# Kernel tuning notes

Measured on AMD Instinct MI355X. Metric: run time of the kernel, lower is better.

Reference implementation:

```python
import jax, jax.numpy as jnp
import numpy as np

N_NODES = 100000
N_EDGES = 3200000
IN_F = 256
OUT_F = 128
NEG_SLOPE = 0.2


def setup_inputs() -> dict:
    key = jax.random.key(0)
    k1, k2, k3, k4, k5 = jax.random.split(key, 5)
    features = jax.random.normal(k1, (N_NODES, IN_F), dtype=jnp.float32)
    # xavier-uniform-ish linear weight [out, in]
    limit = float(np.sqrt(6.0 / (IN_F + OUT_F)))
    weight = jax.random.uniform(k2, (OUT_F, IN_F), dtype=jnp.float32, minval=-limit, maxval=limit)
    edge_vals = jax.random.uniform(k3, (N_EDGES,), dtype=jnp.float32)
    edge_rows = jax.random.randint(k4, (N_EDGES,), 0, N_NODES, dtype=jnp.int32)
    edge_cols = jax.random.randint(k5, (N_EDGES,), 0, N_NODES, dtype=jnp.int32)
    return {"features": features, "weight": weight, "edge_vals": edge_vals,
            "edge_rows": edge_rows, "edge_cols": edge_cols}


def reference(features, weight, edge_vals, edge_rows, edge_cols):
    # support = LeakyReLU(features @ W^T)   (active=True path)
    support = jax.nn.leaky_relu(jnp.einsum('ni,oi->no', features, weight), NEG_SLOPE)
    # output = spmm(adj, support): out[r] += v_e * support[c_e]
    gathered = support[edge_cols] * edge_vals[:, None]   # [E, out]
    out = jax.ops.segment_sum(gathered, edge_rows, num_segments=N_NODES)
    return out
```

## Files before the change

### kernel.cpp

```cpp
#include <hip/hip_runtime.h>
#include <hip/hip_bf16.h>

#define N_NODES 100000
#define N_EDGES 3200000
#define IN_F 256
#define OUT_F 128
#define NEG_SLOPE 0.2f
#define NB 782
#define CHUNK 4096
#define NPB 782
#define BCAP 4608

typedef short s16x8 __attribute__((ext_vector_type(8)));
typedef float f32x4 __attribute__((ext_vector_type(4)));
typedef float f32x2v __attribute__((ext_vector_type(2)));
typedef unsigned u32x2 __attribute__((ext_vector_type(2)));

__device__ __forceinline__ unsigned short f2bf(float f) {
    __bf16 h = (__bf16)f;
    return __builtin_bit_cast(unsigned short, h);
}
__device__ __forceinline__ float bf2f(unsigned short u) {
    unsigned int x = ((unsigned int)u) << 16;
    return __builtin_bit_cast(float, x);
}

__global__ void wcvt_kernel(const float* __restrict__ w, unsigned short* __restrict__ wb) {
    int t = blockIdx.x * blockDim.x + threadIdx.x;
    if (t >= (OUT_F / 16) * (IN_F / 32) * 64) return;
    int lane = t & 63;
    int nt   = (t >> 6) & 7;
    int kit  = t >> 9;
    int l16  = lane & 15;
    int quad = lane >> 4;
    const float* src = w + (nt * 16 + l16) * IN_F + kit * 32 + quad * 8;
    float4 v0 = *(const float4*)src;
    float4 v1 = *(const float4*)(src + 4);
    ushort4 o0, o1;
    o0.x = f2bf(v0.x); o0.y = f2bf(v0.y); o0.z = f2bf(v0.z); o0.w = f2bf(v0.w);
    o1.x = f2bf(v1.x); o1.y = f2bf(v1.y); o1.z = f2bf(v1.z); o1.w = f2bf(v1.w);
    *(ushort4*)(wb + t * 8)     = o0;
    *(ushort4*)(wb + t * 8 + 4) = o1;
}

__global__ __launch_bounds__(256) void gemm_kernel(
    const float* __restrict__ feat, const unsigned short* __restrict__ wb,
    unsigned short* __restrict__ sup) {
    int wid  = threadIdx.x >> 6;
    int lane = threadIdx.x & 63;
    long m0 = ((long)blockIdx.x * 4 + wid) * 16;
    if (m0 >= N_NODES) return;
    int quad = lane >> 4;
    int l16  = lane & 15;
    int kq   = quad * 8;

    const float* arow = feat + (m0 + l16) * IN_F + kq;

    f32x4 acc[8];
#pragma unroll
    for (int nt = 0; nt < 8; ++nt) acc[nt] = (f32x4){0.f, 0.f, 0.f, 0.f};

#pragma unroll
    for (int k0 = 0; k0 < IN_F; k0 += 32) {
        f32x4 a0 = __builtin_nontemporal_load((const f32x4*)(arow + k0));
        f32x4 a1 = __builtin_nontemporal_load((const f32x4*)(arow + k0 + 4));
        s16x8 a;
        a[0] = (short)f2bf(a0[0]); a[1] = (short)f2bf(a0[1]);
        a[2] = (short)f2bf(a0[2]); a[3] = (short)f2bf(a0[3]);
        a[4] = (short)f2bf(a1[0]); a[5] = (short)f2bf(a1[1]);
        a[6] = (short)f2bf(a1[2]); a[7] = (short)f2bf(a1[3]);
        const unsigned short* wp = wb + (k0 >> 5) * 4096 + lane * 8;
#pragma unroll
        for (int nt = 0; nt < 8; ++nt) {
            s16x8 b = *(const s16x8*)(wp + nt * 512);
            acc[nt] = __builtin_amdgcn_mfma_f32_16x16x32_bf16(a, b, acc[nt], 0, 0, 0);
        }
    }

    int crow = (int)m0 + quad * 4;
#pragma unroll
    for (int nt = 0; nt < 8; ++nt) {
#pragma unroll
        for (int r = 0; r < 4; ++r) {
            float v = acc[nt][r];
            v = (v > 0.f) ? v : (NEG_SLOPE * v);
            sup[(long)(crow + r) * OUT_F + nt * 16 + l16] = f2bf(v);
        }
    }
}

__global__ __launch_bounds__(256) void hist_kernel(const int* __restrict__ rows,
                                                   int* __restrict__ gcnt) {
    __shared__ int lh[NB];
    int t = threadIdx.x;
    for (int s = t; s < NB; s += 256) lh[s] = 0;
    __syncthreads();
    int e0 = blockIdx.x * CHUNK;
    int m = N_EDGES - e0; if (m > CHUNK) m = CHUNK;
    for (int k = t; k < m; k += 256)
        atomicAdd(&lh[__builtin_nontemporal_load(rows + e0 + k) >> 7], 1);
    __syncthreads();
    for (int s = t; s < NB; s += 256)
        gcnt[s * NPB + blockIdx.x] = lh[s];
}

__global__ __launch_bounds__(256) void scan_kernel(int* __restrict__ gcnt,
                                                   int* __restrict__ bcnt) {
    __shared__ int st[256];
    int s = blockIdx.x, t = threadIdx.x;
    int* row = gcnt + (long)s * NPB;
    int v[4]; int sum = 0;
#pragma unroll
    for (int k = 0; k < 4; ++k) {
        int i = t * 4 + k;
        v[k] = (i < NPB) ? row[i] : 0;
        sum += v[k];
    }
    st[t] = sum;
    __syncthreads();
    for (int o = 1; o < 256; o <<= 1) {
        int x = (t >= o) ? st[t - o] : 0;
        __syncthreads();
        st[t] += x;
        __syncthreads();
    }
    int run = st[t] - sum;
#pragma unroll
    for (int k = 0; k < 4; ++k) {
        int i = t * 4 + k;
        if (i < NPB) row[i] = run;
        run += v[k];
    }
    if (t == 255) bcnt[s] = run;
}

__global__ __launch_bounds__(256) void mscatter_kernel(const int* __restrict__ rows,
    const int* __restrict__ cols, const float* __restrict__ vals,
    const int* __restrict__ boff, uint2* __restrict__ ed) {
    __shared__ uint2 stage[CHUNK];
    __shared__ unsigned short sbkt[CHUNK];
    __shared__ int lhist[NB];
    __shared__ int lbase[NB];
    __shared__ int st[256];
    int t = threadIdx.x;
    for (int s = t; s < NB; s += 256) lhist[s] = 0;
    __syncthreads();
    int e0 = blockIdx.x * CHUNK;
    int m = N_EDGES - e0; if (m > CHUNK) m = CHUNK;

    int rk[16]; int rr[16]; unsigned cw[16], vw[16];
#pragma unroll
    for (int k = 0; k < 16; ++k) {
        int i = k * 256 + t;
        if (i < m) {
            int e = e0 + i;
            int r = __builtin_nontemporal_load(rows + e);
            rr[k] = r;
            cw[k] = (unsigned)__builtin_nontemporal_load(cols + e);
            vw[k] = __builtin_bit_cast(unsigned, __builtin_nontemporal_load(vals + e));
            rk[k] = atomicAdd(&lhist[r >> 7], 1);
        }
    }
    __syncthreads();
    for (int s = t; s < NB; s += 256)
        lbase[s] = boff[(long)s * NPB + blockIdx.x];
    int base = t * 4; int sum = 0; int hv[4];
#pragma unroll
    for (int k = 0; k < 4; ++k) {
        int s = base + k;
        hv[k] = (s < NB) ? lhist[s] : 0;
        sum += hv[k];
    }
    st[t] = sum;
    __syncthreads();
    for (int o = 1; o < 256; o <<= 1) {
        int x = (t >= o) ? st[t - o] : 0;
        __syncthreads();
        st[t] += x;
        __syncthreads();
    }
    int run = st[t] - sum;
#pragma unroll
    for (int k = 0; k < 4; ++k) {
        int s = base + k;
        if (s < NB) lhist[s] = run;
        run += hv[k];
    }
    __syncthreads();
#pragma unroll
    for (int k = 0; k < 16; ++k) {
        int i = k * 256 + t;
        if (i < m) {
            int r  = rr[k];
            int b  = r >> 7;
            int rl = r & 127;
            int pos = lhist[b] + rk[k];
            stage[pos].x = ((unsigned)rl << 17) | cw[k];
            stage[pos].y = vw[k];
            sbkt[pos] = (unsigned short)b;
        }
    }
    __syncthreads();
    for (int i = t; i < m; i += 256) {
        int b = sbkt[i];
        int g = lbase[b] + (i - lhist[b]);
        if (g < BCAP) ed[(long)b * BCAP + g] = stage[i];
    }
}

__global__ __launch_bounds__(1024) void gather_kernel(const uint2* __restrict__ ed,
    const int* __restrict__ bcnt,
    const unsigned short* __restrict__ sup, float* __restrict__ out, int b0) {
    __shared__ uint2 stage[BCAP];
    __shared__ int h[128];
    __shared__ int bs[128];
    __shared__ int cur[128];
    int t = threadIdx.x;
    int bkt = b0 + blockIdx.x;
    if (t < 128) h[t] = 0;
    __syncthreads();
    int n = bcnt[bkt]; if (n > BCAP) n = BCAP;
    const uint2* p = ed + (long)bkt * BCAP;

    uint2 er[5];
#pragma unroll
    for (int k = 0; k < 5; ++k) {
        int i = k * 1024 + t;
        if (i < n) {
            u32x2 v = __builtin_nontemporal_load((const u32x2*)(p + i));
            er[k].x = v[0]; er[k].y = v[1];
        }
    }
#pragma unroll
    for (int k = 0; k < 5; ++k) {
        int i = k * 1024 + t;
        if (i < n) atomicAdd(&h[er[k].x >> 17], 1);
    }
    __syncthreads();

    if (t < 128) bs[t] = h[t];
    __syncthreads();
    for (int o = 1; o < 128; o <<= 1) {
        int v = 0;
        if (t < 128 && t >= o) v = bs[t - o];
        __syncthreads();
        if (t < 128) bs[t] += v;
        __syncthreads();
    }
    if (t < 128) {
        int excl = bs[t] - h[t];
        bs[t] = excl;
        cur[t] = excl;
    }
    __syncthreads();

#pragma unroll
    for (int k = 0; k < 5; ++k) {
        int i = k * 1024 + t;
        if (i < n) {
            int rl = er[k].x >> 17;
            int pos = atomicAdd(&cur[rl], 1);
            stage[pos] = er[k];
        }
    }
    __syncthreads();

    int wid = t >> 6, lane = t & 63;
    long rowbase = (long)bkt * 128;

#define PROC(E) {                                                            \
        int col = (E).x & 0x1FFFF;                                           \
        float v = __builtin_bit_cast(float, (E).y);                          \
        ushort2 s2 = *(const ushort2*)(sup + (long)col * OUT_F + lane * 2);  \
        a0 += v * bf2f(s2.x); a1 += v * bf2f(s2.y);                          \
    }

    for (int rq = 0; rq < 8; ++rq) {
        int lr = wid * 8 + rq;
        int s0 = bs[lr];
        int mm = h[lr];
        float a0 = 0.f, a1 = 0.f;
        int i = 0;
        for (; i + 16 <= mm; i += 16) {
            uint2 e[16];
#pragma unroll
            for (int k = 0; k < 16; ++k) e[k] = stage[s0 + i + k];
#pragma unroll
            for (int k = 0; k < 16; ++k) PROC(e[k]);
        }
        for (; i + 8 <= mm; i += 8) {
            uint2 e0 = stage[s0 + i],     e1 = stage[s0 + i + 1];
            uint2 e2 = stage[s0 + i + 2], e3 = stage[s0 + i + 3];
            uint2 e4 = stage[s0 + i + 4], e5 = stage[s0 + i + 5];
            uint2 e6 = stage[s0 + i + 6], e7 = stage[s0 + i + 7];
            PROC(e0); PROC(e1); PROC(e2); PROC(e3);
            PROC(e4); PROC(e5); PROC(e6); PROC(e7);
        }
        for (; i < mm; ++i) { uint2 e0 = stage[s0 + i]; PROC(e0); }
        long grow = rowbase + lr;
        if (grow < N_NODES) {
            f32x2v f; f[0] = a0; f[1] = a1;
            __builtin_nontemporal_store(f, (f32x2v*)(out + grow * OUT_F + lane * 2));
        }
    }
#undef PROC
}

extern "C" void kernel_launch(void* const* d_in, const int* in_sizes, int n_in,
                              void* d_out, int out_size, void* d_ws, size_t ws_size,
                              hipStream_t stream) {
    const float* feat  = (const float*)d_in[0];
    const float* w     = (const float*)d_in[1];
    const float* evals = (const float*)d_in[2];
    const int*   erows = (const int*)d_in[3];
    const int*   ecols = (const int*)d_in[4];
    float* out = (float*)d_out;

    char* p = (char*)d_ws;
    unsigned short* wb  = (unsigned short*)p;  p += 65536;
    unsigned short* sup = (unsigned short*)p;  p += (size_t)N_NODES * OUT_F * 2;
    int* gcnt   = (int*)p;                     p += (size_t)NB * NPB * 4;
    int* bcnt   = (int*)p;                     p += 4096;
    uint2* ed   = (uint2*)p;

    wcvt_kernel<<<16, 256, 0, stream>>>(w, wb);

    int gemm_blocks = (N_NODES / 16 + 3) / 4;
    gemm_kernel<<<gemm_blocks, 256, 0, stream>>>(feat, wb, sup);

    hist_kernel<<<NPB, 256, 0, stream>>>(erows, gcnt);
    scan_kernel<<<NB, 256, 0, stream>>>(gcnt, bcnt);
    mscatter_kernel<<<NPB, 256, 0, stream>>>(erows, ecols, evals, gcnt, ed);

    int gh = NB / 2;
    gather_kernel<<<gh, 1024, 0, stream>>>(ed, bcnt, sup, out, 0);
    gather_kernel<<<NB - gh, 1024, 0, stream>>>(ed, bcnt, sup, out, gh);
}
```

Before: 388.4 us.

## Scatter edges directly to global buckets and shrink gather blocks to 512 threads

The multi-scatter kernel drops its shared-memory staging, local scan and second copy pass. Each edge is now written straight to its global bucket slot using its local atomic rank plus the bucket base offset, which removes LDS traffic and several barriers but turns the global writes into uncoalesced scattered stores. Separately, the gather kernel is retuned to 512 threads, with each thread holding 9 edges and each wave covering 16 rows. The gather launch is also split into four launches instead of two.

```diff
diff --git a/kernel.cpp b/kernel.cpp
--- a/kernel.cpp
+++ b/kernel.cpp
@@ -137,11 +137,8 @@
 __global__ __launch_bounds__(256) void mscatter_kernel(const int* __restrict__ rows,
     const int* __restrict__ cols, const float* __restrict__ vals,
     const int* __restrict__ boff, uint2* __restrict__ ed) {
-    __shared__ uint2 stage[CHUNK];
-    __shared__ unsigned short sbkt[CHUNK];
     __shared__ int lhist[NB];
     __shared__ int lbase[NB];
-    __shared__ int st[256];
     int t = threadIdx.x;
     for (int s = t; s < NB; s += 256) lhist[s] = 0;
     __syncthreads();
@@ -164,28 +161,6 @@
     __syncthreads();
     for (int s = t; s < NB; s += 256)
         lbase[s] = boff[(long)s * NPB + blockIdx.x];
-    int base = t * 4; int sum = 0; int hv[4];
-#pragma unroll
-    for (int k = 0; k < 4; ++k) {
-        int s = base + k;
-        hv[k] = (s < NB) ? lhist[s] : 0;
-        sum += hv[k];
-    }
-    st[t] = sum;
-    __syncthreads();
-    for (int o = 1; o < 256; o <<= 1) {
-        int x = (t >= o) ? st[t - o] : 0;
-        __syncthreads();
-        st[t] += x;
-        __syncthreads();
-    }
-    int run = st[t] - sum;
-#pragma unroll
-    for (int k = 0; k < 4; ++k) {
-        int s = base + k;
-        if (s < NB) lhist[s] = run;
-        run += hv[k];
-    }
     __syncthreads();
 #pragma unroll
     for (int k = 0; k < 16; ++k) {
@@ -193,22 +168,18 @@
         if (i < m) {
             int r  = rr[k];
             int b  = r >> 7;
-            int rl = r & 127;
-            int pos = lhist[b] + rk[k];
-            stage[pos].x = ((unsigned)rl << 17) | cw[k];
-            stage[pos].y = vw[k];
-            sbkt[pos] = (unsigned short)b;
-        }
-    }
-    __syncthreads();
-    for (int i = t; i < m; i += 256) {
-        int b = sbkt[i];
-        int g = lbase[b] + (i - lhist[b]);
-        if (g < BCAP) ed[(long)b * BCAP + g] = stage[i];
-    }
-}
-
-__global__ __launch_bounds__(1024) void gather_kernel(const uint2* __restrict__ ed,
+            int g  = lbase[b] + rk[k];
+            if (g < BCAP) {
+                uint2 e;
+                e.x = ((unsigned)(r & 127) << 17) | cw[k];
+                e.y = vw[k];
+                ed[(long)b * BCAP + g] = e;
+            }
+        }
+    }
+}
+
+__global__ __launch_bounds__(512) void gather_kernel(const uint2* __restrict__ ed,
     const int* __restrict__ bcnt,
     const unsigned short* __restrict__ sup, float* __restrict__ out, int b0) {
     __shared__ uint2 stage[BCAP];
@@ -222,18 +193,18 @@
     int n = bcnt[bkt]; if (n > BCAP) n = BCAP;
     const uint2* p = ed + (long)bkt * BCAP;
 
-    uint2 er[5];
-#pragma unroll
-    for (int k = 0; k < 5; ++k) {
-        int i = k * 1024 + t;
+    uint2 er[9];
+#pragma unroll
+    for (int k = 0; k < 9; ++k) {
+        int i = k * 512 + t;
         if (i < n) {
             u32x2 v = __builtin_nontemporal_load((const u32x2*)(p + i));
             er[k].x = v[0]; er[k].y = v[1];
         }
     }
 #pragma unroll
-    for (int k = 0; k < 5; ++k) {
-        int i = k * 1024 + t;
+    for (int k = 0; k < 9; ++k) {
+        int i = k * 512 + t;
         if (i < n) atomicAdd(&h[er[k].x >> 17], 1);
     }
     __syncthreads();
@@ -255,8 +226,8 @@
     __syncthreads();
 
 #pragma unroll
-    for (int k = 0; k < 5; ++k) {
-        int i = k * 1024 + t;
+    for (int k = 0; k < 9; ++k) {
+        int i = k * 512 + t;
         if (i < n) {
             int rl = er[k].x >> 17;
             int pos = atomicAdd(&cur[rl], 1);
@@ -275,8 +246,8 @@
         a0 += v * bf2f(s2.x); a1 += v * bf2f(s2.y);                          \
     }
 
-    for (int rq = 0; rq < 8; ++rq) {
-        int lr = wid * 8 + rq;
+    for (int rq = 0; rq < 16; ++rq) {
+        int lr = wid * 16 + rq;
         int s0 = bs[lr];
         int mm = h[lr];
         float a0 = 0.f, a1 = 0.f;
@@ -332,7 +303,9 @@
     scan_kernel<<<NB, 256, 0, stream>>>(gcnt, bcnt);
     mscatter_kernel<<<NPB, 256, 0, stream>>>(erows, ecols, evals, gcnt, ed);
 
-    int gh = NB / 2;
-    gather_kernel<<<gh, 1024, 0, stream>>>(ed, bcnt, sup, out, 0);
-    gather_kernel<<<NB - gh, 1024, 0, stream>>>(ed, bcnt, sup, out, gh);
-}
+    int q = NB / 4;
+    gather_kernel<<<q, 512, 0, stream>>>(ed, bcnt, sup, out, 0);
+    gather_kernel<<<q, 512, 0, stream>>>(ed, bcnt, sup, out, q);
+    gather_kernel<<<q, 512, 0, stream>>>(ed, bcnt, sup, out, 2 * q);
+    gather_kernel<<<NB - 3 * q, 512, 0, stream>>>(ed, bcnt, sup, out, 3 * q);
+}
```

New measurement: 468.7 us. 20.7% more time.
